# Kernel optimization log

Measured on AMD Instinct MI355X. Metric: run time of the kernel, lower is better.

## Reference

```python
import jax, jax.numpy as jnp
import numpy as np

NUM_NODES = 4096


def _dense_adjs(edge_index, edge_values, n):
    # edge_index: [J, 2, E] int, edge_values: [J, E] float -> [J, n, n]
    # scatter-add == torch_sparse.coalesce (duplicate edges are summed)
    def one(ei, ev):
        return jnp.zeros((n, n), ev.dtype).at[ei[0], ei[1]].add(ev)
    return jax.vmap(one)(edge_index, edge_values)


def setup_inputs() -> dict:
    key = jax.random.key(0)
    k1, k2, k3, k4 = jax.random.split(key, 4)
    J, E, C, N = 5, 150000, 2, NUM_NODES
    edge_index = jax.random.randint(k1, (J, 2, E), 0, N)
    edge_values = jax.random.uniform(k2, (J, E), dtype=jnp.float32)
    w1 = jax.random.normal(k3, (C, J), dtype=jnp.float32) * 0.01
    w2 = jax.random.normal(k4, (C, J), dtype=jnp.float32) * 0.01
    return {"edge_index": edge_index, "edge_values": edge_values, "w1": w1, "w2": w2}


def reference(edge_index, edge_values, w1, w2):
    n = NUM_NODES
    # GTConv: softmax over edge types, weighted sum of per-type adjacencies
    D = _dense_adjs(edge_index, edge_values, n)          # [J, n, n]
    f1 = jax.nn.softmax(w1, axis=1)                      # [C, J]
    f2 = jax.nn.softmax(w2, axis=1)                      # [C, J]
    A1 = jnp.einsum('cj,jmn->cmn', f1, D)                # conv1 output per channel
    A2 = jnp.einsum('cj,jmn->cmn', f2, D)                # conv2 output per channel
    # spspmm per channel == dense matmul of the (zero-padded) sparse matrices
    H = jnp.einsum('cmk,ckn->cmn', A1, A2)               # [C, n, n]
    return (H, f1, f2)
```

## Files before the change

### kernel.cpp

```cpp
#include <hip/hip_runtime.h>
#include <hip/hip_bf16.h>
#include <stdint.h>

#define JT 5
#define NE 150000
#define NC 2
#define NDIM 4096
#define KDIM 4096
#define NNZ (JT * NE)
constexpr size_t MAT = (size_t)NDIM * NDIM;
constexpr size_t HN  = (size_t)NC * MAT;

typedef __bf16 bf16x8 __attribute__((ext_vector_type(8)));
typedef float  f32x4  __attribute__((ext_vector_type(4)));

__global__ void softmax_k(const float* __restrict__ w1, const float* __restrict__ w2,
                          float* __restrict__ fbuf, float* __restrict__ out_tail) {
    int t = threadIdx.x;
    if (t < 2 * NC) {
        const float* w = (t < NC) ? w1 : w2;
        int c = t % NC;
        float v[JT];
        float mx = -1e30f;
        for (int j = 0; j < JT; ++j) { v[j] = w[c * JT + j]; mx = fmaxf(mx, v[j]); }
        float s = 0.f;
        for (int j = 0; j < JT; ++j) { v[j] = expf(v[j] - mx); s += v[j]; }
        float inv = 1.0f / s;
        for (int j = 0; j < JT; ++j) {
            float f = v[j] * inv;
            fbuf[t * JT + j] = f;
            out_tail[t * JT + j] = f;
        }
    }
}

__device__ __forceinline__ void pkadd2(__bf16* p, float lo, float hi) {
    uint16_t a = __builtin_bit_cast(uint16_t, (__bf16)lo);
    uint16_t b = __builtin_bit_cast(uint16_t, (__bf16)hi);
    uint32_t pk = ((uint32_t)b << 16) | a;
    asm volatile("global_atomic_pk_add_bf16 %0, %1, off"
                 :: "v"((uint64_t)(uintptr_t)p), "v"(pk) : "memory");
}

__global__ void scatter2_k(const int* __restrict__ ei, const float* __restrict__ ev,
                           const float* __restrict__ fbuf, __bf16* __restrict__ Xi) {
    int idx = blockIdx.x * blockDim.x + threadIdx.x;
    if (idx >= NNZ) return;
    int j = idx / NE;
    int e = idx - j * NE;
    int r = ei[(size_t)j * 2 * NE + e];
    int c = ei[(size_t)j * 2 * NE + NE + e];
    float v = ev[idx];
    size_t cell = ((size_t)r * NDIM + c) * 4;
    pkadd2(Xi + cell,     fbuf[j]          * v, fbuf[JT + j]     * v);
    pkadd2(Xi + cell + 2, fbuf[2 * JT + j] * v, fbuf[3 * JT + j] * v);
}

__device__ __forceinline__ uint4 gather8(const ushort (*s)[65], int rr, int e8) {
    uint4 v;
    v.x = (uint32_t)s[rr][e8 + 0] | ((uint32_t)s[rr][e8 + 1] << 16);
    v.y = (uint32_t)s[rr][e8 + 2] | ((uint32_t)s[rr][e8 + 3] << 16);
    v.z = (uint32_t)s[rr][e8 + 4] | ((uint32_t)s[rr][e8 + 5] << 16);
    v.w = (uint32_t)s[rr][e8 + 6] | ((uint32_t)s[rr][e8 + 7] << 16);
    return v;
}

__global__ __launch_bounds__(256) void repack_k(const ushort4* __restrict__ Xi,
                                                __bf16* __restrict__ A1,
                                                __bf16* __restrict__ A2T) {
    __shared__ ushort s10[64][65];
    __shared__ ushort s11[64][65];
    __shared__ ushort s20[64][65];
    __shared__ ushort s21[64][65];
    const int r0 = blockIdx.y * 64, c0 = blockIdx.x * 64;
    const int t = threadIdx.x;

#pragma unroll
    for (int it = 0; it < 16; ++it) {
        int li = t + 256 * it;
        int rr = li >> 6, cc = li & 63;
        ushort4 v = Xi[(size_t)(r0 + rr) * NDIM + (c0 + cc)];
        s10[rr][cc] = v.x; s11[rr][cc] = v.y;
        s20[cc][rr] = v.z; s21[cc][rr] = v.w;
    }
    __syncthreads();

#pragma unroll
    for (int a = 0; a < 2; ++a) {
        int w = t + 256 * a;
        int rr = w >> 3, e8 = (w & 7) << 3;
        *(uint4*)(A1 +        (size_t)(r0 + rr) * NDIM + c0 + e8) = gather8(s10, rr, e8);
        *(uint4*)(A1 + MAT +  (size_t)(r0 + rr) * NDIM + c0 + e8) = gather8(s11, rr, e8);
        *(uint4*)(A2T +       (size_t)(c0 + rr) * NDIM + r0 + e8) = gather8(s20, rr, e8);
        *(uint4*)(A2T + MAT + (size_t)(c0 + rr) * NDIM + r0 + e8) = gather8(s21, rr, e8);
    }
}

#define BM 256
#define BN 256
#define BK 64
#define NT (KDIM / BK)

__device__ __forceinline__ void gl_lds16(const __bf16* g, __bf16* l) {
    __builtin_amdgcn_global_load_lds(
        (const __attribute__((address_space(1))) void*)(uintptr_t)g,
        (__attribute__((address_space(3))) void*)l, 16, 0, 0);
}

#define READA(AH) do {                                                            \
    _Pragma("unroll")                                                             \
    for (int i = 0; i < 4; ++i)                                                   \
        _Pragma("unroll")                                                         \
        for (int ks = 0; ks < 2; ++ks)                                            \
            af[i][ks] = *(const bf16x8*)(ldsAc + (AH) * 16384 +                   \
                ((((rAl + i * 16) * 128) + ks * 64 + kb) ^ swz));                 \
} while (0)

#define READB(BH) do {                                                            \
    _Pragma("unroll")                                                             \
    for (int n = 0; n < 2; ++n)                                                   \
        _Pragma("unroll")                                                         \
        for (int ks = 0; ks < 2; ++ks)                                            \
            bf_[n][ks] = *(const bf16x8*)(ldsBc + (BH) * 16384 +                  \
                ((((rBl + n * 16) * 128) + ks * 64 + kb) ^ swz));                 \
} while (0)

#define MFMA16(AH, BH) do {                                                       \
    asm volatile("s_waitcnt lgkmcnt(0)" ::: "memory");                            \
    __builtin_amdgcn_s_setprio(1);                                                \
    _Pragma("unroll")                                                             \
    for (int i = 0; i < 4; ++i)                                                   \
        _Pragma("unroll")                                                         \
        for (int n = 0; n < 2; ++n)                                               \
            _Pragma("unroll")                                                     \
            for (int ks = 0; ks < 2; ++ks)                                        \
                acc[AH][BH][i][n] = __builtin_amdgcn_mfma_f32_16x16x32_bf16(      \
                    af[i][ks], bf_[n][ks], acc[AH][BH][i][n], 0, 0, 0);           \
    __builtin_amdgcn_s_setprio(0);                                                \
} while (0)

#define GATE_BAR(N) do {                                                          \
    asm volatile("s_waitcnt vmcnt(" #N ")" ::: "memory");                         \
    __builtin_amdgcn_s_barrier();                                                 \
    asm volatile("" ::: "memory");                                                \
} while (0)

__global__ __launch_bounds__(512, 2) void gemm_k(const __bf16* __restrict__ A,
                                                 const __bf16* __restrict__ B,
                                                 float* __restrict__ C) {
    __shared__ __align__(16) __bf16 sm[65536];

    const int u    = threadIdx.x;
    const int lane = u & 63;
    const int wv   = u >> 6;
    const int wr   = (wv >> 2) * 64;
    const int wc   = (wv & 3) * 32;
    const size_t matoff = (size_t)blockIdx.z * MAT;
    const size_t brow   = (size_t)blockIdx.y * BM;
    const size_t bcol   = (size_t)blockIdx.x * BN;

    const int srow = u >> 3;
    const int kc   = (u & 7) ^ (srow & 7);
    const __bf16* Ab = A + matoff + (brow + srow) * KDIM + kc * 8;
    const __bf16* Bb = B + matoff + (bcol + srow) * KDIM + kc * 8;
    char* const smb = (char*)sm;

    auto stage = [&](int mat, int h, int tt) {
        const __bf16* base = mat ? Bb : Ab;
#pragma unroll
        for (int unit = 0; unit < 2; ++unit) {
            const __bf16* src = base + (size_t)(h * 128 + unit * 64) * KDIM + (size_t)tt * BK;
            __bf16* dst = (__bf16*)(smb + (tt & 1) * 65536 + mat * 32768 +
                                    h * 16384 + unit * 8192 + wv * 1024);
            gl_lds16(src, dst);
        }
    };

    const int rAl = wr + (lane & 15);
    const int rBl = wc + (lane & 15);
    const int kb  = (lane >> 4) * 16;
    const int swz = (lane & 7) << 4;

    f32x4 acc[2][2][4][2];
#pragma unroll
    for (int a = 0; a < 2; ++a)
#pragma unroll
        for (int b = 0; b < 2; ++b)
#pragma unroll
            for (int i = 0; i < 4; ++i)
#pragma unroll
                for (int n = 0; n < 2; ++n) acc[a][b][i][n] = (f32x4){0.f, 0.f, 0.f, 0.f};

    bf16x8 af[4][2], bf_[2][2];

    stage(0, 0, 0); stage(1, 0, 0); stage(1, 1, 0); stage(0, 1, 0);

    for (int t = 0; t < NT - 1; ++t) {
        const char* ldsAc = smb + (t & 1) * 65536;
        const char* ldsBc = ldsAc + 32768;
        const int nxt = t + 1;
        GATE_BAR(4);
        stage(0, 0, nxt);
        READA(0); READB(0);
        MFMA16(0, 0);
        GATE_BAR(4);
        stage(1, 0, nxt);
        READB(1);
        MFMA16(0, 1);
        GATE_BAR(4);
        stage(1, 1, nxt);
        READA(1);
        MFMA16(1, 1);
        stage(0, 1, nxt);
        READB(0);
        MFMA16(1, 0);
    }
    {
        const char* ldsAc = smb + ((NT - 1) & 1) * 65536;
        const char* ldsBc = ldsAc + 32768;
        GATE_BAR(4);
        READA(0); READB(0);
        MFMA16(0, 0);
        GATE_BAR(2);
        READB(1);
        MFMA16(0, 1);
        GATE_BAR(0);
        READA(1);
        MFMA16(1, 1);
        READB(0);
        MFMA16(1, 0);
    }

    float* Cc = C + matoff;
#pragma unroll
    for (int a = 0; a < 2; ++a)
#pragma unroll
        for (int b = 0; b < 2; ++b)
#pragma unroll
            for (int i = 0; i < 4; ++i) {
                int orow0 = (int)brow + a * 128 + wr + i * 16 + (lane >> 4) * 4;
#pragma unroll
                for (int n = 0; n < 2; ++n) {
                    int ocol = (int)bcol + b * 128 + wc + n * 16 + (lane & 15);
                    float* p = Cc + (size_t)orow0 * NDIM + ocol;
#pragma unroll
                    for (int jj = 0; jj < 4; ++jj) p[(size_t)jj * NDIM] = acc[a][b][i][n][jj];
                }
            }
}

extern "C" void kernel_launch(void* const* d_in, const int* in_sizes, int n_in,
                              void* d_out, int out_size, void* d_ws, size_t ws_size,
                              hipStream_t stream) {
    const int*   ei = (const int*)d_in[0];
    const float* ev = (const float*)d_in[1];
    const float* w1 = (const float*)d_in[2];
    const float* w2 = (const float*)d_in[3];
    float* out = (float*)d_out;

    char* ws = (char*)d_ws;
    __bf16* A1b  = (__bf16*)ws;
    __bf16* A2b  = (__bf16*)(ws + HN * sizeof(__bf16));
    float*  fbuf = (float*)(ws + 2 * HN * sizeof(__bf16));
    size_t needed = 2 * HN * sizeof(__bf16) + 32 * sizeof(float);
    if (ws_size < needed) return;

    __bf16* Xi = (__bf16*)d_out;

    softmax_k<<<dim3(1), dim3(64), 0, stream>>>(w1, w2, fbuf, out + HN);

    hipMemsetAsync(Xi, 0, HN * sizeof(float), stream);

    const int nb = (NNZ + 255) / 256;
    scatter2_k<<<dim3(nb), dim3(256), 0, stream>>>(ei, ev, fbuf, Xi);

    repack_k<<<dim3(64, 64), dim3(256), 0, stream>>>((const ushort4*)Xi, A1b, A2b);

    gemm_k<<<dim3(NDIM / BN, NDIM / BM, NC), dim3(512), 0, stream>>>(A1b, A2b, out);
}
```

Measured before the change: 338.5 us.

## Load B fragments directly from global into registers, keep only A in LDS

Restructures the GEMM main loop so the B operand is loaded straight from global memory into double-buffered register fragments (even/odd sets), while only A is staged through LDS. LDS use drops from 128 KB to 64 KB per block and the B-side LDS writes, reads and the associated barrier are gone. The vmcnt gating is retuned for the mixed LDS-DMA and register loads. In exchange each lane issues uncoalesced strided 16-byte global loads for B (rows KDIM apart), register pressure rises with two B fragment sets, and global-load latency is now exposed directly to the MFMA operands.

```diff
diff --git a/kernel.cpp b/kernel.cpp
--- a/kernel.cpp
+++ b/kernel.cpp
@@ -107,25 +107,40 @@
         (__attribute__((address_space(3))) void*)l, 16, 0, 0);
 }
 
-#define READA(AH) do {                                                            \
+#define GATE_(N) asm volatile("s_waitcnt vmcnt(" #N ")" ::: "memory")
+#define GATE(N) GATE_(N)
+#define FENCE asm volatile("" ::: "memory")
+
+#define STAGEA(H, TT) do {                                                        \
+    _Pragma("unroll")                                                             \
+    for (int unit = 0; unit < 2; ++unit) {                                        \
+        const __bf16* src = Ab + (size_t)((H) * 128 + unit * 64) * KDIM           \
+                               + (size_t)(TT) * BK;                               \
+        __bf16* dst = (__bf16*)(smb + ((TT) & 1) * 32768 + (H) * 16384            \
+                                + unit * 8192 + wv * 1024);                       \
+        gl_lds16(src, dst);                                                       \
+    }                                                                             \
+} while (0)
+
+#define LOADB(DST, BH, TT) do {                                                   \
+    _Pragma("unroll")                                                             \
+    for (int n = 0; n < 2; ++n)                                                   \
+        _Pragma("unroll")                                                         \
+        for (int ks = 0; ks < 2; ++ks)                                            \
+            DST[BH][n][ks] = *(const bf16x8*)(Bc +                                \
+                (size_t)((BH) * 128 + n * 16) * KDIM + (size_t)(TT) * BK + ks * 32); \
+} while (0)
+
+#define READA(H) do {                                                             \
     _Pragma("unroll")                                                             \
     for (int i = 0; i < 4; ++i)                                                   \
         _Pragma("unroll")                                                         \
         for (int ks = 0; ks < 2; ++ks)                                            \
-            af[i][ks] = *(const bf16x8*)(ldsAc + (AH) * 16384 +                   \
+            af[i][ks] = *(const bf16x8*)(ldsA + (H) * 16384 +                     \
                 ((((rAl + i * 16) * 128) + ks * 64 + kb) ^ swz));                 \
 } while (0)
 
-#define READB(BH) do {                                                            \
-    _Pragma("unroll")                                                             \
-    for (int n = 0; n < 2; ++n)                                                   \
-        _Pragma("unroll")                                                         \
-        for (int ks = 0; ks < 2; ++ks)                                            \
-            bf_[n][ks] = *(const bf16x8*)(ldsBc + (BH) * 16384 +                  \
-                ((((rBl + n * 16) * 128) + ks * 64 + kb) ^ swz));                 \
-} while (0)
-
-#define MFMA16(AH, BH) do {                                                       \
+#define MFMA16(AH, BH, BSET) do {                                                 \
     asm volatile("s_waitcnt lgkmcnt(0)" ::: "memory");                            \
     __builtin_amdgcn_s_setprio(1);                                                \
     _Pragma("unroll")                                                             \
@@ -135,20 +150,35 @@
             _Pragma("unroll")                                                     \
             for (int ks = 0; ks < 2; ++ks)                                        \
                 acc[AH][BH][i][n] = __builtin_amdgcn_mfma_f32_16x16x32_bf16(      \
-                    af[i][ks], bf_[n][ks], acc[AH][BH][i][n], 0, 0, 0);           \
+                    af[i][ks], BSET[BH][n][ks], acc[AH][BH][i][n], 0, 0, 0);      \
     __builtin_amdgcn_s_setprio(0);                                                \
 } while (0)
 
-#define GATE_BAR(N) do {                                                          \
-    asm volatile("s_waitcnt vmcnt(" #N ")" ::: "memory");                         \
+#define TILE(T, BCUR, BNXT, HN, G0, G1, G2) do {                                  \
+    const char* ldsA = smb + ((T) & 1) * 32768;                                   \
+    GATE(G0);                                                                     \
     __builtin_amdgcn_s_barrier();                                                 \
-    asm volatile("" ::: "memory");                                                \
+    FENCE;                                                                        \
+    if (HN) { STAGEA(0, (T) + 1); LOADB(BNXT, 0, (T) + 1); }                      \
+    READA(0);                                                                     \
+    MFMA16(0, 0, BCUR);                                                           \
+    GATE(G1);                                                                     \
+    FENCE;                                                                        \
+    if (HN) { LOADB(BNXT, 1, (T) + 1); }                                          \
+    MFMA16(0, 1, BCUR);                                                           \
+    GATE(G2);                                                                     \
+    __builtin_amdgcn_s_barrier();                                                 \
+    FENCE;                                                                        \
+    if (HN) { STAGEA(1, (T) + 1); }                                               \
+    READA(1);                                                                     \
+    MFMA16(1, 1, BCUR);                                                           \
+    MFMA16(1, 0, BCUR);                                                           \
 } while (0)
 
 __global__ __launch_bounds__(512, 2) void gemm_k(const __bf16* __restrict__ A,
                                                  const __bf16* __restrict__ B,
                                                  float* __restrict__ C) {
-    __shared__ __align__(16) __bf16 sm[65536];
+    __shared__ __align__(16) __bf16 sm[2 * 16384];
 
     const int u    = threadIdx.x;
     const int lane = u & 63;
@@ -162,22 +192,12 @@
     const int srow = u >> 3;
     const int kc   = (u & 7) ^ (srow & 7);
     const __bf16* Ab = A + matoff + (brow + srow) * KDIM + kc * 8;
-    const __bf16* Bb = B + matoff + (bcol + srow) * KDIM + kc * 8;
     char* const smb = (char*)sm;
 
-    auto stage = [&](int mat, int h, int tt) {
-        const __bf16* base = mat ? Bb : Ab;
-#pragma unroll
-        for (int unit = 0; unit < 2; ++unit) {
-            const __bf16* src = base + (size_t)(h * 128 + unit * 64) * KDIM + (size_t)tt * BK;
-            __bf16* dst = (__bf16*)(smb + (tt & 1) * 65536 + mat * 32768 +
-                                    h * 16384 + unit * 8192 + wv * 1024);
-            gl_lds16(src, dst);
-        }
-    };
+    const __bf16* Bc = B + matoff + (bcol + wc + (size_t)(lane & 15)) * KDIM
+                         + ((lane >> 4) << 3);
 
     const int rAl = wr + (lane & 15);
-    const int rBl = wc + (lane & 15);
     const int kb  = (lane >> 4) * 16;
     const int swz = (lane & 7) << 4;
 
@@ -191,45 +211,20 @@
 #pragma unroll
                 for (int n = 0; n < 2; ++n) acc[a][b][i][n] = (f32x4){0.f, 0.f, 0.f, 0.f};
 
-    bf16x8 af[4][2], bf_[2][2];
-
-    stage(0, 0, 0); stage(1, 0, 0); stage(1, 1, 0); stage(0, 1, 0);
-
-    for (int t = 0; t < NT - 1; ++t) {
-        const char* ldsAc = smb + (t & 1) * 65536;
-        const char* ldsBc = ldsAc + 32768;
-        const int nxt = t + 1;
-        GATE_BAR(4);
-        stage(0, 0, nxt);
-        READA(0); READB(0);
-        MFMA16(0, 0);
-        GATE_BAR(4);
-        stage(1, 0, nxt);
-        READB(1);
-        MFMA16(0, 1);
-        GATE_BAR(4);
-        stage(1, 1, nxt);
-        READA(1);
-        MFMA16(1, 1);
-        stage(0, 1, nxt);
-        READB(0);
-        MFMA16(1, 0);
-    }
-    {
-        const char* ldsAc = smb + ((NT - 1) & 1) * 65536;
-        const char* ldsBc = ldsAc + 32768;
-        GATE_BAR(4);
-        READA(0); READB(0);
-        MFMA16(0, 0);
-        GATE_BAR(2);
-        READB(1);
-        MFMA16(0, 1);
-        GATE_BAR(0);
-        READA(1);
-        MFMA16(1, 1);
-        READB(0);
-        MFMA16(1, 0);
-    }
+    bf16x8 af[4][2];
+    bf16x8 bE[2][2][2], bO[2][2][2];
+
+    STAGEA(0, 0);
+    LOADB(bE, 0, 0);
+    LOADB(bE, 1, 0);
+    STAGEA(1, 0);
+
+    for (int t = 0; t < NT - 2; t += 2) {
+        TILE(t,     bE, bO, true, 6, 8, 10);
+        TILE(t + 1, bO, bE, true, 6, 8, 10);
+    }
+    TILE(NT - 2, bE, bO, true,  6, 8, 10);
+    TILE(NT - 1, bO, bE, false, 6, 2, 0);
 
     float* Cc = C + matoff;
 #pragma unroll
```

Result: slower. 481.7 us (+42.3%).
